# Optimization experiments

Hardware: AMD Instinct MI355X
Metric: run time of the kernel (lower is better)

## Reference

```python
import jax, jax.numpy as jnp
from jax import lax
import numpy as np


def _hat(w):
    wx, wy, wz = w[0], w[1], w[2]
    z = jnp.zeros((), w.dtype)
    return jnp.array([[z, -wz, wy], [wz, z, -wx], [-wy, wx, z]])


def _se3_exp(x):
    # x[:3] = so3 rotation vector, x[3:] = translation part of the twist
    w, v = x[:3], x[3:]
    t2 = jnp.sum(w * w)
    small = t2 < 1e-8
    th = jnp.sqrt(jnp.where(small, 1.0, t2))
    A = jnp.where(small, 1.0 - t2 / 6.0, jnp.sin(th) / th)
    B = jnp.where(small, 0.5 - t2 / 24.0, (1.0 - jnp.cos(th)) / (th * th))
    C = jnp.where(small, 1.0 / 6.0 - t2 / 120.0, (th - jnp.sin(th)) / (th * th * th))
    W = _hat(w)
    W2 = W @ W
    I = jnp.eye(3, dtype=x.dtype)
    R = I + A * W + B * W2
    V = I + B * W + C * W2
    t = V @ v
    return R, t


def _sobel_grads(img):
    # matches torch: valid conv, crop inner border, zero-pad by 2 -> [H, W]
    sob = jnp.array([[-0.125, -0.25, -0.125], [0.0, 0.0, 0.0], [0.125, 0.25, 0.125]], img.dtype)
    x4 = img[None, None]  # NCHW
    gx = lax.conv_general_dilated(x4, sob.T[None, None], (1, 1), 'VALID')[0, 0]
    gy = lax.conv_general_dilated(x4, sob[None, None], (1, 1), 'VALID')[0, 0]
    crop_pad = lambda g: jnp.pad(g[1:-1, 1:-1], 2)
    return crop_pad(gx), crop_pad(gy)


def _j_wt(pts, fx):
    # per-point 2x6 jacobian of pixel coords w.r.t. se3 twist (as in the torch code,
    # which uses intrinsics[0,0] for both rows)
    xp, yp, zp = pts[:, 0], pts[:, 1], pts[:, 2]
    zi = 1.0 / zp
    zi2 = zi * zi
    zero = jnp.zeros_like(zi)
    r0 = jnp.stack([-fx * xp * yp * zi2, fx * (1.0 + xp * xp * zi2), -fx * yp * zi,
                    fx * zi, zero, -fx * xp * zi2], axis=-1)
    r1 = jnp.stack([-fx * (1.0 + yp * yp * zi2), fx * xp * yp * zi2, fx * xp * zi,
                    zero, fx * zi, -fx * yp * zi2], axis=-1)
    return jnp.stack([r0, r1], axis=1)  # (N, 2, 6)


def _forward(x, ref_img, ref_depth, trg_img, intrinsics):
    H, W = ref_img.shape
    fx, fy = intrinsics[0, 0], intrinsics[1, 1]
    cx, cy = intrinsics[0, 2], intrinsics[1, 2]
    # back-project ref_depth to a point cloud (one point per pixel)
    vv, uu = jnp.meshgrid(jnp.arange(H, dtype=ref_img.dtype),
                          jnp.arange(W, dtype=ref_img.dtype), indexing='ij')
    z = ref_depth.ravel()
    pts = jnp.stack([(uu.ravel() - cx) * z / fx, (vv.ravel() - cy) * z / fy, z], axis=1)  # (N,3)
    # transform + project
    R, t = _se3_exp(x)
    p = pts @ R.T + t  # (N,3)
    proj = p @ intrinsics.T
    uw = proj[:, 0] / proj[:, 2]
    vw = proj[:, 1] / proj[:, 2]
    ui = uw.astype(jnp.int32)  # truncation toward zero, like torch .long()
    vi = vw.astype(jnp.int32)
    valid = (vi < H) & (ui < W) & (vi > 0) & (ui > 0)
    flat = jnp.clip(vi, 0, H - 1) * W + jnp.clip(ui, 0, W - 1)
    warped = ref_img.ravel()[flat]  # gather warp
    residuals = jnp.where(valid, warped - trg_img.ravel(), 0.0)  # (N,)
    # image jacobian of target image, then chain with per-point 2x6 jacobian
    gx, gy = _sobel_grads(trg_img)
    J_img = jnp.stack([gx.ravel(), gy.ravel()], axis=-1)  # (N,2)
    Jw = _j_wt(pts, fx)  # (N,2,6)
    J = jnp.einsum('nk,nkj->nj', J_img, Jw)  # (N,6)
    J = jnp.where(valid[:, None], J, 0.0)
    return jnp.concatenate([residuals[:, None], J], axis=1)  # (N,7)


def setup_inputs() -> dict:
    key = jax.random.key(0)
    k1, k2, k3 = jax.random.split(key, 3)
    H, W = 1080, 1920
    ref_img = jax.random.uniform(k1, (H, W), dtype=jnp.float32)
    trg_img = jax.random.uniform(k2, (H, W), dtype=jnp.float32)
    ref_depth = 1.0 + 4.0 * jax.random.uniform(k3, (H, W), dtype=jnp.float32)  # depth in [1,5]
    x = jnp.zeros((6,), dtype=jnp.float32)  # LM initial pose
    intrinsics = jnp.array([[1000.0, 0.0, 960.0], [0.0, 1000.0, 540.0], [0.0, 0.0, 1.0]],
                           dtype=jnp.float32)
    return {'x': x, 'ref_img': ref_img, 'ref_depth': ref_depth,
            'trg_img': trg_img, 'intrinsics': intrinsics}


def reference(x, ref_img, ref_depth, trg_img, intrinsics):
    return _forward(x, ref_img, ref_depth, trg_img, intrinsics)
```

## Files before the change

### kernel.cpp

```cpp
#include <hip/hip_runtime.h>
#include <cmath>

#define IMG_H 1080
#define IMG_W 1920
#define NPIX (IMG_H * IMG_W)
#define BLOCK 256
#define NBLOCKS (NPIX / BLOCK)

__global__ __launch_bounds__(BLOCK) void pose_fwd_kernel(
    const float* __restrict__ x,
    const float* __restrict__ ref_img,
    const float* __restrict__ ref_depth,
    const float* __restrict__ trg_img,
    const float* __restrict__ K,
    float* __restrict__ out)
{
    __shared__ float sRt[12];
    __shared__ float sout[BLOCK * 7];

    const int tid = threadIdx.x;

    if (tid == 0) {
        const float wx = x[0], wy = x[1], wz = x[2];
        const float vx = x[3], vy = x[4], vz = x[5];
        const float t2 = wx * wx + wy * wy + wz * wz;
        float A, B, C;
        if (t2 < 1e-8f) {
            A = 1.0f - t2 / 6.0f;
            B = 0.5f - t2 / 24.0f;
            C = 1.0f / 6.0f - t2 / 120.0f;
        } else {
            const float th = sqrtf(t2);
            const float s = sinf(th), c = cosf(th);
            A = s / th;
            B = (1.0f - c) / t2;
            C = (th - s) / (t2 * th);
        }
        const float W00 = -(wy * wy + wz * wz), W01 = wx * wy, W02 = wx * wz;
        const float W11 = -(wx * wx + wz * wz), W12 = wy * wz;
        const float W22 = -(wx * wx + wy * wy);
        sRt[0] = 1.0f + B * W00;        sRt[1] = A * (-wz) + B * W01;  sRt[2] = A * wy + B * W02;
        sRt[3] = A * wz + B * W01;      sRt[4] = 1.0f + B * W11;       sRt[5] = A * (-wx) + B * W12;
        sRt[6] = A * (-wy) + B * W02;   sRt[7] = A * wx + B * W12;     sRt[8] = 1.0f + B * W22;
        const float V00 = 1.0f + C * W00,      V01 = B * (-wz) + C * W01, V02 = B * wy + C * W02;
        const float V10 = B * wz + C * W01,    V11 = 1.0f + C * W11,      V12 = B * (-wx) + C * W12;
        const float V20 = B * (-wy) + C * W02, V21 = B * wx + C * W12,    V22 = 1.0f + C * W22;
        sRt[9]  = V00 * vx + V01 * vy + V02 * vz;
        sRt[10] = V10 * vx + V11 * vy + V12 * vz;
        sRt[11] = V20 * vx + V21 * vy + V22 * vz;
    }
    __syncthreads();

    const unsigned n = blockIdx.x * BLOCK + tid;
    const int v = (int)(n / IMG_W);
    const int u = (int)(n - (unsigned)v * IMG_W);

    const float k00 = K[0], k01 = K[1], k02 = K[2];
    const float k10 = K[3], k11 = K[4], k12 = K[5];
    const float k20 = K[6], k21 = K[7], k22 = K[8];
    const float fx = k00, fy = k11, cx = k02, cy = k12;

    const float z = ref_depth[n];
    const float X = ((float)u - cx) * z / fx;
    const float Y = ((float)v - cy) * z / fy;

    const float R0 = sRt[0], R1 = sRt[1], R2 = sRt[2];
    const float R3 = sRt[3], R4 = sRt[4], R5 = sRt[5];
    const float R6 = sRt[6], R7 = sRt[7], R8 = sRt[8];
    const float tx = sRt[9], ty = sRt[10], tz = sRt[11];

    const float px = R0 * X + R1 * Y + R2 * z + tx;
    const float py = R3 * X + R4 * Y + R5 * z + ty;
    const float pz = R6 * X + R7 * Y + R8 * z + tz;

    const float p0 = k00 * px + k01 * py + k02 * pz;
    const float p1 = k10 * px + k11 * py + k12 * pz;
    const float p2 = k20 * px + k21 * py + k22 * pz;

    const float uw = p0 / p2;
    const float vw = p1 / p2;
    const int ui = (int)uw;
    const int vi = (int)vw;
    const bool valid = (vi < IMG_H) && (ui < IMG_W) && (vi > 0) && (ui > 0);
    const int cu = min(max(ui, 0), IMG_W - 1);
    const int cv = min(max(vi, 0), IMG_H - 1);
    const float warped = ref_img[cv * IMG_W + cu];
    const float res = valid ? (warped - trg_img[n]) : 0.0f;

    float gx = 0.0f, gy = 0.0f;
    if (v >= 2 && v <= IMG_H - 3 && u >= 2 && u <= IMG_W - 3) {
        const float* tp = trg_img + (size_t)(v - 1) * IMG_W + (u - 1);
        const float t00 = tp[0],          t01 = tp[1],          t02 = tp[2];
        const float t10 = tp[IMG_W],                            t12 = tp[IMG_W + 2];
        const float t20 = tp[2 * IMG_W],  t21 = tp[2 * IMG_W + 1], t22 = tp[2 * IMG_W + 2];
        gx = 0.125f * (t02 - t00) + 0.25f * (t12 - t10) + 0.125f * (t22 - t20);
        gy = 0.125f * (t20 - t00) + 0.25f * (t21 - t01) + 0.125f * (t22 - t02);
    }

    const float zi = 1.0f / z;
    const float zi2 = zi * zi;
    const float fzi = fx * zi;
    float J0 = 0.0f, J1 = 0.0f, J2 = 0.0f, J3 = 0.0f, J4 = 0.0f, J5 = 0.0f;
    if (valid) {
        const float xy = X * Y * zi2;
        J0 = gx * (-fx * xy)                 + gy * (-fx * (1.0f + Y * Y * zi2));
        J1 = gx * ( fx * (1.0f + X * X * zi2)) + gy * ( fx * xy);
        J2 = gx * (-fx * Y * zi)             + gy * ( fx * X * zi);
        J3 = gx * fzi;
        J4 = gy * fzi;
        J5 = gx * (-fx * X * zi2)            + gy * (-fx * Y * zi2);
    }

    sout[tid * 7 + 0] = res;
    sout[tid * 7 + 1] = J0;
    sout[tid * 7 + 2] = J1;
    sout[tid * 7 + 3] = J2;
    sout[tid * 7 + 4] = J3;
    sout[tid * 7 + 5] = J4;
    sout[tid * 7 + 6] = J5;
    __syncthreads();

    const int base = blockIdx.x * (BLOCK * 7);
#pragma unroll
    for (int j = 0; j < 7; ++j) {
        out[base + j * BLOCK + tid] = sout[j * BLOCK + tid];
    }
}

extern "C" void kernel_launch(void* const* d_in, const int* in_sizes, int n_in,
                              void* d_out, int out_size, void* d_ws, size_t ws_size,
                              hipStream_t stream) {
    const float* x          = (const float*)d_in[0];
    const float* ref_img    = (const float*)d_in[1];
    const float* ref_depth  = (const float*)d_in[2];
    const float* trg_img    = (const float*)d_in[3];
    const float* intrinsics = (const float*)d_in[4];
    float* out = (float*)d_out;

    pose_fwd_kernel<<<NBLOCKS, BLOCK, 0, stream>>>(
        x, ref_img, ref_depth, trg_img, intrinsics, out);
}
```

Measured before the change: 23.75 us.

## Process four pixels per thread with vectorized stencil loads and float4 stores

Each thread now handles four consecutive pixels. It loads depth and nine float4 chunks of the target-image rows once and reuses them for the Sobel stencil and the residuals, and it writes results through float4 shared-memory and global stores. Divisions are replaced with hardware reciprocal approximations. This cuts per-pixel load instructions and index arithmetic, at the cost of a quarter as many blocks, more registers, and slightly less accurate reciprocals.

```diff
diff --git a/kernel.cpp b/kernel.cpp
--- a/kernel.cpp
+++ b/kernel.cpp
@@ -5,7 +5,9 @@
 #define IMG_W 1920
 #define NPIX (IMG_H * IMG_W)
 #define BLOCK 256
-#define NBLOCKS (NPIX / BLOCK)
+#define PXT 4
+#define PXB (BLOCK * PXT)
+#define NBLOCKS (NPIX / PXB)
 
 __global__ __launch_bounds__(BLOCK) void pose_fwd_kernel(
     const float* __restrict__ x,
@@ -16,7 +18,7 @@
     float* __restrict__ out)
 {
     __shared__ float sRt[12];
-    __shared__ float sout[BLOCK * 7];
+    __shared__ float sout[PXB * 7];
 
     const int tid = threadIdx.x;
 
@@ -51,79 +53,123 @@
     }
     __syncthreads();
 
-    const unsigned n = blockIdx.x * BLOCK + tid;
-    const int v = (int)(n / IMG_W);
-    const int u = (int)(n - (unsigned)v * IMG_W);
+    const int n0 = blockIdx.x * PXB + tid * PXT;
+    const int v  = n0 / IMG_W;
+    const int u0 = n0 - v * IMG_W;
 
     const float k00 = K[0], k01 = K[1], k02 = K[2];
     const float k10 = K[3], k11 = K[4], k12 = K[5];
     const float k20 = K[6], k21 = K[7], k22 = K[8];
     const float fx = k00, fy = k11, cx = k02, cy = k12;
-
-    const float z = ref_depth[n];
-    const float X = ((float)u - cx) * z / fx;
-    const float Y = ((float)v - cy) * z / fy;
+    const float inv_fx = __builtin_amdgcn_rcpf(fx);
+    const float inv_fy = __builtin_amdgcn_rcpf(fy);
 
     const float R0 = sRt[0], R1 = sRt[1], R2 = sRt[2];
     const float R3 = sRt[3], R4 = sRt[4], R5 = sRt[5];
     const float R6 = sRt[6], R7 = sRt[7], R8 = sRt[8];
     const float tx = sRt[9], ty = sRt[10], tz = sRt[11];
 
-    const float px = R0 * X + R1 * Y + R2 * z + tx;
-    const float py = R3 * X + R4 * Y + R5 * z + ty;
-    const float pz = R6 * X + R7 * Y + R8 * z + tz;
+    const float4 dz4 = *(const float4*)(ref_depth + n0);
+    const float zs[4] = {dz4.x, dz4.y, dz4.z, dz4.w};
 
-    const float p0 = k00 * px + k01 * py + k02 * pz;
-    const float p1 = k10 * px + k11 * py + k12 * pz;
-    const float p2 = k20 * px + k21 * py + k22 * pz;
+    const int rm1 = (v > 0)         ? v - 1 : 0;
+    const int rp1 = (v < IMG_H - 1) ? v + 1 : IMG_H - 1;
+    const int cl  = (u0 > 0)            ? u0 - 4 : 0;
+    const int cr  = (u0 + 8 <= IMG_W)   ? u0 + 4 : IMG_W - 4;
 
-    const float uw = p0 / p2;
-    const float vw = p1 / p2;
-    const int ui = (int)uw;
-    const int vi = (int)vw;
-    const bool valid = (vi < IMG_H) && (ui < IMG_W) && (vi > 0) && (ui > 0);
-    const int cu = min(max(ui, 0), IMG_W - 1);
-    const int cv = min(max(vi, 0), IMG_H - 1);
-    const float warped = ref_img[cv * IMG_W + cu];
-    const float res = valid ? (warped - trg_img[n]) : 0.0f;
+    const float* rtop = trg_img + (size_t)rm1 * IMG_W;
+    const float* rmid = trg_img + (size_t)v   * IMG_W;
+    const float* rbot = trg_img + (size_t)rp1 * IMG_W;
 
-    float gx = 0.0f, gy = 0.0f;
-    if (v >= 2 && v <= IMG_H - 3 && u >= 2 && u <= IMG_W - 3) {
-        const float* tp = trg_img + (size_t)(v - 1) * IMG_W + (u - 1);
-        const float t00 = tp[0],          t01 = tp[1],          t02 = tp[2];
-        const float t10 = tp[IMG_W],                            t12 = tp[IMG_W + 2];
-        const float t20 = tp[2 * IMG_W],  t21 = tp[2 * IMG_W + 1], t22 = tp[2 * IMG_W + 2];
-        gx = 0.125f * (t02 - t00) + 0.25f * (t12 - t10) + 0.125f * (t22 - t20);
-        gy = 0.125f * (t20 - t00) + 0.25f * (t21 - t01) + 0.125f * (t22 - t02);
+    const float4 ta = *(const float4*)(rtop + cl);
+    const float4 tb = *(const float4*)(rtop + u0);
+    const float4 tc = *(const float4*)(rtop + cr);
+    const float4 ma = *(const float4*)(rmid + cl);
+    const float4 mb = *(const float4*)(rmid + u0);
+    const float4 mc = *(const float4*)(rmid + cr);
+    const float4 ba = *(const float4*)(rbot + cl);
+    const float4 bb = *(const float4*)(rbot + u0);
+    const float4 bc = *(const float4*)(rbot + cr);
+
+    const float top[6] = {ta.w, tb.x, tb.y, tb.z, tb.w, tc.x};
+    const float mid[6] = {ma.w, mb.x, mb.y, mb.z, mb.w, mc.x};
+    const float bot[6] = {ba.w, bb.x, bb.y, bb.z, bb.w, bc.x};
+
+    const bool vok = (v >= 2) && (v <= IMG_H - 3);
+    const float vf = (float)v;
+
+    float out_local[28];
+
+#pragma unroll
+    for (int j = 0; j < PXT; ++j) {
+        const float z = zs[j];
+        const float uf = (float)(u0 + j);
+        const float X = (uf - cx) * z * inv_fx;
+        const float Y = (vf - cy) * z * inv_fy;
+
+        const float px = fmaf(R0, X, fmaf(R1, Y, fmaf(R2, z, tx)));
+        const float py = fmaf(R3, X, fmaf(R4, Y, fmaf(R5, z, ty)));
+        const float pz = fmaf(R6, X, fmaf(R7, Y, fmaf(R8, z, tz)));
+
+        const float p0 = fmaf(k00, px, fmaf(k01, py, k02 * pz));
+        const float p1 = fmaf(k10, px, fmaf(k11, py, k12 * pz));
+        const float p2 = fmaf(k20, px, fmaf(k21, py, k22 * pz));
+
+        const float rp2 = __builtin_amdgcn_rcpf(p2);
+        const float uw = p0 * rp2;
+        const float vw = p1 * rp2;
+        const int ui = (int)uw;
+        const int vi = (int)vw;
+        const bool valid = (vi < IMG_H) && (ui < IMG_W) && (vi > 0) && (ui > 0);
+        const int cu = min(max(ui, 0), IMG_W - 1);
+        const int cv = min(max(vi, 0), IMG_H - 1);
+        const float warped = ref_img[cv * IMG_W + cu];
+        const float res = valid ? (warped - mid[j + 1]) : 0.0f;
+
+        float gx = 0.0f, gy = 0.0f;
+        if (vok && (u0 + j >= 2) && (u0 + j <= IMG_W - 3)) {
+            gx = 0.125f * (top[j + 2] - top[j]) + 0.25f * (mid[j + 2] - mid[j])
+               + 0.125f * (bot[j + 2] - bot[j]);
+            gy = 0.125f * (bot[j] - top[j]) + 0.25f * (bot[j + 1] - top[j + 1])
+               + 0.125f * (bot[j + 2] - top[j + 2]);
+        }
+
+        float J0 = 0.0f, J1 = 0.0f, J2 = 0.0f, J3 = 0.0f, J4 = 0.0f, J5 = 0.0f;
+        if (valid) {
+            const float zi  = __builtin_amdgcn_rcpf(z);
+            const float zi2 = zi * zi;
+            const float xy  = X * Y * zi2;
+            const float gxfx = gx * fx, gyfx = gy * fx;
+            J0 = -gxfx * xy - gyfx * fmaf(Y * Y, zi2, 1.0f);
+            J1 =  gxfx * fmaf(X * X, zi2, 1.0f) + gyfx * xy;
+            J2 = (gyfx * X - gxfx * Y) * zi;
+            J3 =  gxfx * zi;
+            J4 =  gyfx * zi;
+            J5 = -(gxfx * X + gyfx * Y) * zi2;
+        }
+
+        out_local[j * 7 + 0] = res;
+        out_local[j * 7 + 1] = J0;
+        out_local[j * 7 + 2] = J1;
+        out_local[j * 7 + 3] = J2;
+        out_local[j * 7 + 4] = J3;
+        out_local[j * 7 + 5] = J4;
+        out_local[j * 7 + 6] = J5;
     }
 
-    const float zi = 1.0f / z;
-    const float zi2 = zi * zi;
-    const float fzi = fx * zi;
-    float J0 = 0.0f, J1 = 0.0f, J2 = 0.0f, J3 = 0.0f, J4 = 0.0f, J5 = 0.0f;
-    if (valid) {
-        const float xy = X * Y * zi2;
-        J0 = gx * (-fx * xy)                 + gy * (-fx * (1.0f + Y * Y * zi2));
-        J1 = gx * ( fx * (1.0f + X * X * zi2)) + gy * ( fx * xy);
-        J2 = gx * (-fx * Y * zi)             + gy * ( fx * X * zi);
-        J3 = gx * fzi;
-        J4 = gy * fzi;
-        J5 = gx * (-fx * X * zi2)            + gy * (-fx * Y * zi2);
+    float4* sout4 = (float4*)sout;
+#pragma unroll
+    for (int q = 0; q < 7; ++q) {
+        sout4[tid * 7 + q] = make_float4(out_local[q * 4 + 0], out_local[q * 4 + 1],
+                                         out_local[q * 4 + 2], out_local[q * 4 + 3]);
     }
-
-    sout[tid * 7 + 0] = res;
-    sout[tid * 7 + 1] = J0;
-    sout[tid * 7 + 2] = J1;
-    sout[tid * 7 + 3] = J2;
-    sout[tid * 7 + 4] = J3;
-    sout[tid * 7 + 5] = J4;
-    sout[tid * 7 + 6] = J5;
     __syncthreads();
 
-    const int base = blockIdx.x * (BLOCK * 7);
+    const float4* src4 = (const float4*)sout;
+    float4* out4 = (float4*)out + (size_t)blockIdx.x * (PXB * 7 / 4);
 #pragma unroll
-    for (int j = 0; j < 7; ++j) {
-        out[base + j * BLOCK + tid] = sout[j * BLOCK + tid];
+    for (int q = 0; q < 7; ++q) {
+        out4[q * BLOCK + tid] = src4[q * BLOCK + tid];
     }
 }
 
```

Result: slower. 24.45 us (+3.0%).
